# Kernel tuning notes

Hardware: AMD Instinct MI355X
Metric: run time of the kernel (lower is better)

The kernel has to match this reference:

```python
import jax, jax.numpy as jnp
import numpy as np

S, D, E = 8192, 128, 48  # seq_len, embedding_dim, num pos tags (experts)

def setup_inputs() -> dict:
    key = jax.random.key(0)
    ks = jax.random.split(key, 8)
    sc = 1.0 / np.sqrt(D)
    return {
        "embs": jax.random.normal(ks[0], (S, D), dtype=jnp.float32),
        "pos_ids": jax.random.randint(ks[1], (S,), 0, E),
        "W_exp": jax.random.normal(ks[2], (E, D, D), dtype=jnp.float32) * sc,
        "b_exp": jax.random.normal(ks[3], (E, D), dtype=jnp.float32) * sc,
        "W_ih": jax.random.normal(ks[4], (4 * D, D), dtype=jnp.float32) * sc,
        "W_hh": jax.random.normal(ks[5], (4 * D, D), dtype=jnp.float32) * sc,
        "b_ih": jax.random.normal(ks[6], (4 * D,), dtype=jnp.float32) * sc,
        "b_hh": jax.random.normal(ks[7], (4 * D,), dtype=jnp.float32) * sc,
    }

def reference(embs, pos_ids, W_exp, b_exp, W_ih, W_hh, b_ih, b_hh):
    d = embs.shape[1]
    # --- per-token expert Linear (pos-tag-routed) ---
    # gather expert weights per token: [S, D, D], then per-token GEMV
    Wg = W_exp[pos_ids]                      # [S, D, D]
    bg = b_exp[pos_ids]                      # [S, D]
    z = jnp.einsum('sij,sj->si', Wg, embs) + bg  # [S, D]
    # --- 1-layer LSTM (PyTorch gate order: i, f, g, o) ---
    x_gates = z @ W_ih.T + b_ih + b_hh       # [S, 4D], precompute input contribution
    def step(carry, xg):
        h, c = carry
        gates = xg + h @ W_hh.T              # [4D]
        i, f, g, o = jnp.split(gates, 4)
        i = jax.nn.sigmoid(i)
        f = jax.nn.sigmoid(f)
        g = jnp.tanh(g)
        o = jax.nn.sigmoid(o)
        c = f * c + i * g
        h = o * jnp.tanh(c)
        return (h, c), h
    h0 = jnp.zeros((d,), dtype=embs.dtype)
    c0 = jnp.zeros((d,), dtype=embs.dtype)
    _, hs = jax.lax.scan(step, (h0, c0), x_gates)  # hs: [S, D]
    # --- max-pool over time; batch dim of 1 as in the torch module ---
    out = jnp.max(hs, axis=0)[None, :]       # [1, D]
    return out
```

## Files before the change

kernel.cpp:

```cpp
#include <hip/hip_runtime.h>
#include <math.h>


#define SEQ   8192
#define DIM   128
#define NGATE 512
#define NEXP  48

typedef _Float16 v8h  __attribute__((ext_vector_type(8)));
typedef float    v4f  __attribute__((ext_vector_type(4)));

__device__ __forceinline__ float sigm_fast(float x) {
    return __fdividef(1.0f, 1.0f + __expf(-x));
}
__device__ __forceinline__ float tanh_fast(float x) {
    float e = __expf(2.0f * x);
    return 1.0f - __fdividef(2.0f, e + 1.0f);
}
__device__ __forceinline__ v8h pack8(float4 a, float4 b) {
    v8h r;
    r[0]=(_Float16)a.x; r[1]=(_Float16)a.y; r[2]=(_Float16)a.z; r[3]=(_Float16)a.w;
    r[4]=(_Float16)b.x; r[5]=(_Float16)b.y; r[6]=(_Float16)b.z; r[7]=(_Float16)b.w;
    return r;
}
__device__ __forceinline__ float selv(v4f A, v4f B, int c) {
    float a01 = (c & 1) ? A[1] : A[0];
    float a23 = (c & 1) ? A[3] : A[2];
    float av  = (c & 2) ? a23 : a01;
    float b01 = (c & 1) ? B[1] : B[0];
    float b23 = (c & 1) ? B[3] : B[2];
    float bv  = (c & 2) ? b23 : b01;
    return (c & 4) ? bv : av;
}

__global__ __launch_bounds__(64) void expert_gemv(
    const float* __restrict__ embs, const int* __restrict__ pos_ids,
    const float* __restrict__ W_exp, const float* __restrict__ b_exp,
    float* __restrict__ xg)
{
    __shared__ float Wl[DIM * DIM];
    const int e     = blockIdx.x % NEXP;
    const int slice = blockIdx.x / NEXP;
    const int tid   = threadIdx.x;

    const float4* Wg = (const float4*)(W_exp + (size_t)e * DIM * DIM);
    #pragma unroll 4
    for (int it = 0; it < 64; ++it) {
        int idx = it * 64 + tid;
        int r = idx >> 5, c4 = idx & 31;
        float4 v = Wg[idx];
        *(float4*)&Wl[r * DIM + (((c4 ^ (r & 31))) << 2)] = v;
    }
    const float b0 = b_exp[e * DIM + tid];
    const float b1 = b_exp[e * DIM + 64 + tid];
    __syncthreads();

    const int r0 = tid, r1 = tid + 64;
    const int sw0 = r0 & 31, sw1 = r1 & 31;
    const int sBeg = slice * 1024, sEnd = sBeg + 1024;
    for (int base = sBeg; base < sEnd; base += 64) {
        int pid = pos_ids[base + tid];
        unsigned long long m = __ballot(pid == e);
        while (m) {
            int t = __builtin_ctzll(m);
            m &= m - 1;
            int s = base + t;
            const float4* ev = (const float4*)(embs + (size_t)s * DIM);
            float a0 = b0, a1 = b1;
            #pragma unroll
            for (int j4 = 0; j4 < 32; ++j4) {
                float4 x  = ev[j4];
                float4 w0 = *(const float4*)&Wl[r0 * DIM + ((j4 ^ sw0) << 2)];
                float4 w1 = *(const float4*)&Wl[r1 * DIM + ((j4 ^ sw1) << 2)];
                a0 = fmaf(w0.x,x.x,fmaf(w0.y,x.y,fmaf(w0.z,x.z,fmaf(w0.w,x.w,a0))));
                a1 = fmaf(w1.x,x.x,fmaf(w1.y,x.y,fmaf(w1.z,x.z,fmaf(w1.w,x.w,a1))));
            }
            float* zp = xg + (size_t)s * NGATE;
            zp[tid]      = a0;
            zp[tid + 64] = a1;
        }
    }
}

__global__ __launch_bounds__(256) void gate_gemm(
    const float* __restrict__ W_ih, const float* __restrict__ b_ih,
    const float* __restrict__ b_hh, float* __restrict__ xg)
{
    __shared__ float zl[32 * DIM];
    __shared__ float Wl[64 * DIM];
    const int tid = threadIdx.x;
    const int s0  = blockIdx.x * 32;

    #pragma unroll
    for (int it = 0; it < 4; ++it) {
        int idx = it * 256 + tid;
        int tok = idx >> 5, c4 = idx & 31;
        float4 v = *(const float4*)(xg + ((size_t)(s0 + tok)) * NGATE + (c4 << 2));
        *(float4*)&zl[tok * DIM + (((c4 ^ (tok & 31))) << 2)] = v;
    }
    __syncthreads();

    const int lane = tid & 63;
    const int tg   = tid >> 6;
    const int swr  = lane & 31;

    for (int ch = 0; ch < 8; ++ch) {
        #pragma unroll
        for (int it = 0; it < 8; ++it) {
            int idx = it * 256 + tid;
            int r = idx >> 5, c4 = idx & 31;
            float4 v = *(const float4*)(W_ih + ((size_t)(ch * 64 + r)) * DIM + (c4 << 2));
            *(float4*)&Wl[r * DIM + ((c4 ^ (r & 31)) << 2)] = v;
        }
        __syncthreads();

        const int row = ch * 64 + lane;
        const float bias = b_ih[row] + b_hh[row];
        float acc[8];
        #pragma unroll
        for (int k = 0; k < 8; ++k) acc[k] = bias;
        #pragma unroll 8
        for (int j4 = 0; j4 < 32; ++j4) {
            float4 w = *(const float4*)&Wl[lane * DIM + ((j4 ^ swr) << 2)];
            #pragma unroll
            for (int k = 0; k < 8; ++k) {
                int tok = tg * 8 + k;
                float4 z = *(const float4*)&zl[tok * DIM + ((j4 ^ (tok & 31)) << 2)];
                acc[k] = fmaf(w.x,z.x,fmaf(w.y,z.y,fmaf(w.z,z.z,fmaf(w.w,z.w,acc[k]))));
            }
        }
        const int pidx = ((row & 127) << 2) + (row >> 7);
        #pragma unroll
        for (int k = 0; k < 8; ++k) {
            int tok = tg * 8 + k;
            xg[((size_t)(s0 + tok)) * NGATE + pidx] = acc[k];
        }
        __syncthreads();
    }
}

__global__ __launch_bounds__(256, 1) void lstm_scan(
    const float* __restrict__ xg, const float* __restrict__ W_hh,
    float* __restrict__ out)
{
    const int T    = threadIdx.x;
    const int wg   = T >> 6;
    const int lane = T & 63;
    const int q    = lane >> 4;
    const int c    = lane & 15;
    const int q8   = q * 8;
    const bool upd = (c < 8);
    const int d    = wg * 32 + q * 4 + (c & 3) + ((c & 4) ? 16 : 0);

    __shared__ __align__(16) _Float16 hbuf[2][DIM];

#define LOADA(G,H) \
    v8h a##G##H##0, a##G##H##1, a##G##H##2, a##G##H##3; { \
        const float4* p = (const float4*)(W_hh + \
            (size_t)((G) * 128 + wg * 32 + (H) * 16 + c) * DIM) + q * 2; \
        a##G##H##0 = pack8(p[ 0], p[ 1]); \
        a##G##H##1 = pack8(p[ 8], p[ 9]); \
        a##G##H##2 = pack8(p[16], p[17]); \
        a##G##H##3 = pack8(p[24], p[25]); }
    LOADA(0,0) LOADA(0,1) LOADA(1,0) LOADA(1,1)
    LOADA(2,0) LOADA(2,1) LOADA(3,0) LOADA(3,1)
#undef LOADA

    float cst  = 0.0f;
    float hmax = -INFINITY;

    if (upd) hbuf[0][d] = (_Float16)0.0f;
    __syncthreads();

    float4 X0 = {0,0,0,0}, X1 = X0, X2 = X0, X3 = X0;
    if (upd) {
        X0 = *(const float4*)(xg + (size_t)0 * NGATE + 4 * d);
        X1 = *(const float4*)(xg + (size_t)1 * NGATE + 4 * d);
        X2 = *(const float4*)(xg + (size_t)2 * NGATE + 4 * d);
        X3 = *(const float4*)(xg + (size_t)3 * NGATE + 4 * d);
    }

    const v4f Z4 = {0.0f, 0.0f, 0.0f, 0.0f};

#define MFMA4(G,H,B0,B1,B2,B3) \
    __builtin_amdgcn_mfma_f32_16x16x32_f16(a##G##H##3, B3, \
    __builtin_amdgcn_mfma_f32_16x16x32_f16(a##G##H##2, B2, \
    __builtin_amdgcn_mfma_f32_16x16x32_f16(a##G##H##1, B1, \
    __builtin_amdgcn_mfma_f32_16x16x32_f16(a##G##H##0, B0, Z4, 0,0,0), 0,0,0), 0,0,0), 0,0,0)

#define STEP(XV, tp, bf, nbf) { \
    const v8h B0 = *(const v8h*)&hbuf[bf][ 0 + q8]; \
    const v8h B1 = *(const v8h*)&hbuf[bf][32 + q8]; \
    const v8h B2 = *(const v8h*)&hbuf[bf][64 + q8]; \
    const v8h B3 = *(const v8h*)&hbuf[bf][96 + q8]; \
    float4 xcur = XV; \
    if (upd) XV = *(const float4*)(xg + (size_t)(tp) * NGATE + 4 * d); \
    v4f acc00 = MFMA4(0,0,B0,B1,B2,B3); v4f acc01 = MFMA4(0,1,B0,B1,B2,B3); \
    v4f acc10 = MFMA4(1,0,B0,B1,B2,B3); v4f acc11 = MFMA4(1,1,B0,B1,B2,B3); \
    v4f acc20 = MFMA4(2,0,B0,B1,B2,B3); v4f acc21 = MFMA4(2,1,B0,B1,B2,B3); \
    v4f acc30 = MFMA4(3,0,B0,B1,B2,B3); v4f acc31 = MFMA4(3,1,B0,B1,B2,B3); \
    if (upd) { \
        const float pi = selv(acc00, acc01, c) + xcur.x; \
        const float pf = selv(acc10, acc11, c) + xcur.y; \
        const float pg = selv(acc20, acc21, c) + xcur.z; \
        const float po = selv(acc30, acc31, c) + xcur.w; \
        const float iv = sigm_fast(pi); \
        const float fv = sigm_fast(pf); \
        const float gv = tanh_fast(pg); \
        const float ov = sigm_fast(po); \
        cst = fmaf(fv, cst, iv * gv); \
        const float h = ov * tanh_fast(cst); \
        hmax = fmaxf(hmax, h); \
        hbuf[nbf][d] = (_Float16)h; \
    } \
    asm volatile("s_waitcnt lgkmcnt(0)\n\ts_barrier" ::: "memory"); }

    for (int t = 0; t < SEQ; t += 4) {
        const int t4 = (t + 4 < SEQ) ? t + 4 : SEQ - 1;
        const int t5 = (t + 5 < SEQ) ? t + 5 : SEQ - 1;
        const int t6 = (t + 6 < SEQ) ? t + 6 : SEQ - 1;
        const int t7 = (t + 7 < SEQ) ? t + 7 : SEQ - 1;
        STEP(X0, t4, 0, 1)
        STEP(X1, t5, 1, 0)
        STEP(X2, t6, 0, 1)
        STEP(X3, t7, 1, 0)
    }
#undef STEP
#undef MFMA4

    if (upd) out[d] = hmax;
}

extern "C" void kernel_launch(void* const* d_in, const int* in_sizes, int n_in,
                              void* d_out, int out_size, void* d_ws, size_t ws_size,
                              hipStream_t stream)
{
    const float* embs  = (const float*)d_in[0];
    const int*   pos   = (const int*)  d_in[1];
    const float* W_exp = (const float*)d_in[2];
    const float* b_exp = (const float*)d_in[3];
    const float* W_ih  = (const float*)d_in[4];
    const float* W_hh  = (const float*)d_in[5];
    const float* b_ih  = (const float*)d_in[6];
    const float* b_hh  = (const float*)d_in[7];
    float* out = (float*)d_out;
    float* xg  = (float*)d_ws;

    expert_gemv<<<dim3(NEXP * 8), 64, 0, stream>>>(embs, pos, W_exp, b_exp, xg);
    gate_gemm  <<<dim3(256), 256, 0, stream>>>(W_ih, b_ih, b_hh, xg);
    lstm_scan  <<<dim3(1), 256, 0, stream>>>(xg, W_hh, out);
}
```

Measured before the change: 5.034 ms.

## Split LSTM scan across 8 wavefronts and interleave independent MFMA chains

The single-block LSTM recurrence now uses 512 threads (8 waves), each owning 16 hidden units instead of 32, which halves the per-wave MFMA count per timestep. The four gate MFMA chains are interleaved so independent accumulators issue back to back instead of serial dependent chains. The selection logic simplifies to a 4-way select. In exchange the per-step barrier covers twice as many waves and fewer lanes per wave do the elementwise gate math.

```diff
diff --git a/kernel.cpp b/kernel.cpp
--- a/kernel.cpp
+++ b/kernel.cpp
@@ -23,14 +23,10 @@
     r[4]=(_Float16)b.x; r[5]=(_Float16)b.y; r[6]=(_Float16)b.z; r[7]=(_Float16)b.w;
     return r;
 }
-__device__ __forceinline__ float selv(v4f A, v4f B, int c) {
-    float a01 = (c & 1) ? A[1] : A[0];
-    float a23 = (c & 1) ? A[3] : A[2];
-    float av  = (c & 2) ? a23 : a01;
-    float b01 = (c & 1) ? B[1] : B[0];
-    float b23 = (c & 1) ? B[3] : B[2];
-    float bv  = (c & 2) ? b23 : b01;
-    return (c & 4) ? bv : av;
+__device__ __forceinline__ float sel4(v4f A, int c) {
+    float v01 = (c & 1) ? A[1] : A[0];
+    float v23 = (c & 1) ? A[3] : A[2];
+    return (c & 2) ? v23 : v01;
 }
 
 __global__ __launch_bounds__(64) void expert_gemv(
@@ -139,31 +135,30 @@
     }
 }
 
-__global__ __launch_bounds__(256, 1) void lstm_scan(
+__global__ __launch_bounds__(512, 2) void lstm_scan(
     const float* __restrict__ xg, const float* __restrict__ W_hh,
     float* __restrict__ out)
 {
     const int T    = threadIdx.x;
-    const int wg   = T >> 6;
+    const int w    = T >> 6;
     const int lane = T & 63;
     const int q    = lane >> 4;
     const int c    = lane & 15;
     const int q8   = q * 8;
-    const bool upd = (c < 8);
-    const int d    = wg * 32 + q * 4 + (c & 3) + ((c & 4) ? 16 : 0);
+    const bool upd = (c < 4);
+    const int d    = w * 16 + q * 4 + c;
 
     __shared__ __align__(16) _Float16 hbuf[2][DIM];
 
-#define LOADA(G,H) \
-    v8h a##G##H##0, a##G##H##1, a##G##H##2, a##G##H##3; { \
+#define LOADA(G) \
+    v8h a##G##_0, a##G##_1, a##G##_2, a##G##_3; { \
         const float4* p = (const float4*)(W_hh + \
-            (size_t)((G) * 128 + wg * 32 + (H) * 16 + c) * DIM) + q * 2; \
-        a##G##H##0 = pack8(p[ 0], p[ 1]); \
-        a##G##H##1 = pack8(p[ 8], p[ 9]); \
-        a##G##H##2 = pack8(p[16], p[17]); \
-        a##G##H##3 = pack8(p[24], p[25]); }
-    LOADA(0,0) LOADA(0,1) LOADA(1,0) LOADA(1,1)
-    LOADA(2,0) LOADA(2,1) LOADA(3,0) LOADA(3,1)
+            (size_t)((G) * 128 + w * 16 + c) * DIM) + q * 2; \
+        a##G##_0 = pack8(p[ 0], p[ 1]); \
+        a##G##_1 = pack8(p[ 8], p[ 9]); \
+        a##G##_2 = pack8(p[16], p[17]); \
+        a##G##_3 = pack8(p[24], p[25]); }
+    LOADA(0) LOADA(1) LOADA(2) LOADA(3)
 #undef LOADA
 
     float cst  = 0.0f;
@@ -182,11 +177,7 @@
 
     const v4f Z4 = {0.0f, 0.0f, 0.0f, 0.0f};
 
-#define MFMA4(G,H,B0,B1,B2,B3) \
-    __builtin_amdgcn_mfma_f32_16x16x32_f16(a##G##H##3, B3, \
-    __builtin_amdgcn_mfma_f32_16x16x32_f16(a##G##H##2, B2, \
-    __builtin_amdgcn_mfma_f32_16x16x32_f16(a##G##H##1, B1, \
-    __builtin_amdgcn_mfma_f32_16x16x32_f16(a##G##H##0, B0, Z4, 0,0,0), 0,0,0), 0,0,0), 0,0,0)
+#define MF(G,K,B,CIN) __builtin_amdgcn_mfma_f32_16x16x32_f16(a##G##_##K, B, CIN, 0, 0, 0)
 
 #define STEP(XV, tp, bf, nbf) { \
     const v8h B0 = *(const v8h*)&hbuf[bf][ 0 + q8]; \
@@ -195,15 +186,17 @@
     const v8h B3 = *(const v8h*)&hbuf[bf][96 + q8]; \
     float4 xcur = XV; \
     if (upd) XV = *(const float4*)(xg + (size_t)(tp) * NGATE + 4 * d); \
-    v4f acc00 = MFMA4(0,0,B0,B1,B2,B3); v4f acc01 = MFMA4(0,1,B0,B1,B2,B3); \
-    v4f acc10 = MFMA4(1,0,B0,B1,B2,B3); v4f acc11 = MFMA4(1,1,B0,B1,B2,B3); \
-    v4f acc20 = MFMA4(2,0,B0,B1,B2,B3); v4f acc21 = MFMA4(2,1,B0,B1,B2,B3); \
-    v4f acc30 = MFMA4(3,0,B0,B1,B2,B3); v4f acc31 = MFMA4(3,1,B0,B1,B2,B3); \
+     \
+    v4f c0 = MF(0,0,B0,Z4);  v4f c1 = MF(1,0,B0,Z4); \
+    v4f c2 = MF(2,0,B0,Z4);  v4f c3 = MF(3,0,B0,Z4); \
+    c0 = MF(0,1,B1,c0);  c1 = MF(1,1,B1,c1);  c2 = MF(2,1,B1,c2);  c3 = MF(3,1,B1,c3); \
+    c0 = MF(0,2,B2,c0);  c1 = MF(1,2,B2,c1);  c2 = MF(2,2,B2,c2);  c3 = MF(3,2,B2,c3); \
+    c0 = MF(0,3,B3,c0);  c1 = MF(1,3,B3,c1);  c2 = MF(2,3,B3,c2);  c3 = MF(3,3,B3,c3); \
     if (upd) { \
-        const float pi = selv(acc00, acc01, c) + xcur.x; \
-        const float pf = selv(acc10, acc11, c) + xcur.y; \
-        const float pg = selv(acc20, acc21, c) + xcur.z; \
-        const float po = selv(acc30, acc31, c) + xcur.w; \
+        const float pi = sel4(c0, c) + xcur.x; \
+        const float pf = sel4(c1, c) + xcur.y; \
+        const float pg = sel4(c2, c) + xcur.z; \
+        const float po = sel4(c3, c) + xcur.w; \
         const float iv = sigm_fast(pi); \
         const float fv = sigm_fast(pf); \
         const float gv = tanh_fast(pg); \
@@ -226,7 +219,7 @@
         STEP(X3, t7, 1, 0)
     }
 #undef STEP
-#undef MFMA4
+#undef MF
 
     if (upd) out[d] = hmax;
 }
@@ -248,5 +241,5 @@
 
     expert_gemv<<<dim3(NEXP * 8), 64, 0, stream>>>(embs, pos, W_exp, b_exp, xg);
     gate_gemm  <<<dim3(256), 256, 0, stream>>>(W_ih, b_ih, b_hh, xg);
-    lstm_scan  <<<dim3(1), 256, 0, stream>>>(xg, W_hh, out);
-}
+    lstm_scan  <<<dim3(1), 512, 0, stream>>>(xg, W_hh, out);
+}
```

Result: slower. 5.327 ms (+5.8%).
